# Kernel tuning notes

Hardware: AMD Instinct MI355X
Metric: run time of the kernel (lower is better)

## Reference

```python
import jax, jax.numpy as jnp
import numpy as np
from jax import lax

D_MODEL = 1024
D_STATE = 16
D_CONV = 4
EXPAND = 2
D_INNER = EXPAND * D_MODEL            # 2048
DT_RANK = (D_MODEL + 15) // 16        # 64
B, L = 2, 2048
EPS = 1e-5


def setup_inputs() -> dict:
    key = jax.random.key(0)
    ks = jax.random.split(key, 12)
    s = 0.02
    x = jax.random.normal(ks[0], (B, L, D_MODEL), dtype=jnp.float32)
    norm_w = jnp.ones((D_MODEL,), dtype=jnp.float32)
    in_proj_w = jax.random.normal(ks[1], (2 * D_INNER, D_MODEL), dtype=jnp.float32) * s
    conv_w = jax.random.normal(ks[2], (D_INNER, D_CONV), dtype=jnp.float32) * 0.1
    conv_b = jax.random.normal(ks[3], (D_INNER,), dtype=jnp.float32) * 0.01
    x_proj_w = jax.random.normal(ks[4], (DT_RANK + 2 * D_STATE, D_INNER), dtype=jnp.float32) * s
    dt_proj_w = jax.random.normal(ks[5], (D_INNER, DT_RANK), dtype=jnp.float32) * 0.1
    dt_proj_b = jax.random.normal(ks[6], (D_INNER,), dtype=jnp.float32) * 0.5 - 4.0  # small softplus(delta)
    # S4D-real init: A = -(1..d_state) per channel
    A_log = jnp.log(jnp.broadcast_to(jnp.arange(1, D_STATE + 1, dtype=jnp.float32), (D_INNER, D_STATE)))
    Dp = jnp.ones((D_INNER,), dtype=jnp.float32)
    out_proj_w = jax.random.normal(ks[7], (D_MODEL, D_INNER), dtype=jnp.float32) * s
    return {"x": x, "norm_w": norm_w, "in_proj_w": in_proj_w, "conv_w": conv_w,
            "conv_b": conv_b, "x_proj_w": x_proj_w, "dt_proj_w": dt_proj_w,
            "dt_proj_b": dt_proj_b, "A_log": A_log, "Dp": Dp, "out_proj_w": out_proj_w}


def _selective_scan(deltaA, deltaBu, Cm):
    # deltaA, deltaBu: [B,L,Di,N]; Cm: [B,L,N] -> y: [B,L,Di]
    def step(h, inp):
        dA, dBu, c = inp
        h = dA * h + dBu                       # [B,Di,N]
        y = jnp.einsum('bdn,bn->bd', h, c)     # [B,Di]
        return h, y
    h0 = jnp.zeros(deltaA.shape[0:1] + deltaA.shape[2:], deltaA.dtype)
    _, ys = lax.scan(step, h0, (deltaA.transpose(1, 0, 2, 3),
                                deltaBu.transpose(1, 0, 2, 3),
                                Cm.transpose(1, 0, 2)))
    return ys.transpose(1, 0, 2)               # [B,L,Di]


def reference(x, norm_w, in_proj_w, conv_w, conv_b, x_proj_w,
              dt_proj_w, dt_proj_b, A_log, Dp, out_proj_w):
    d_inner, d_conv = conv_w.shape
    d_state = A_log.shape[1]
    dt_rank = dt_proj_w.shape[1]

    # RMSNorm
    rms = jnp.sqrt(jnp.mean(x * x, axis=-1, keepdims=True) + EPS)
    xn = norm_w * (x / rms)

    # input projection -> x, z streams
    xz = jnp.einsum('bld,ed->ble', xn, in_proj_w)      # [B,L,2*Di]
    xi, z = jnp.split(xz, 2, axis=-1)

    # depthwise causal conv1d + SiLU
    xc = lax.conv_general_dilated(
        xi.transpose(0, 2, 1), conv_w[:, None, :], (1,), [(d_conv - 1, 0)],
        dimension_numbers=('NCL', 'OIL', 'NCL'), feature_group_count=d_inner)
    xc = jax.nn.silu(xc.transpose(0, 2, 1) + conv_b)   # [B,L,Di]

    # input-dependent SSM params
    dbl = jnp.einsum('bld,ed->ble', xc, x_proj_w)      # [B,L,dt_rank+2N]
    dt, Bm, Cm = jnp.split(dbl, [dt_rank, dt_rank + d_state], axis=-1)
    delta = jax.nn.softplus(jnp.einsum('blr,dr->bld', dt, dt_proj_w) + dt_proj_b)

    A = -jnp.exp(A_log)                                # [Di,N]
    deltaA = jnp.exp(delta[..., None] * A)             # [B,L,Di,N]
    deltaBu = delta[..., None] * Bm[:, :, None, :] * xc[..., None]

    y = _selective_scan(deltaA, deltaBu, Cm)           # [B,L,Di]
    y = y + xc * Dp
    y = y * jax.nn.silu(z)

    out = jnp.einsum('bld,ed->ble', y, out_proj_w)     # [B,L,d_model]
    return x + out
```

## Files before the change

kernel.cpp:

```cpp
#include <hip/hip_runtime.h>
#include <hip/hip_bf16.h>
#include <math.h>

#define D_MODEL 1024
#define D_STATE 16
#define D_CONV 4
#define D_INNER 2048
#define DT_RANK 64
#define BATCH 2
#define SEQ 2048
#define NTOK (BATCH*SEQ)
#define EPS 1e-5f
#define CCH 32
#define TCH (SEQ/CCH)
#define XKS 8
#define XKC (D_INNER/XKS)

typedef __attribute__((ext_vector_type(8))) short short8;
typedef __attribute__((ext_vector_type(4))) float f32x4;
typedef __attribute__((ext_vector_type(4))) unsigned short us4;

__device__ inline unsigned short f2bf(float f) {
  union { __hip_bfloat16 h; unsigned short u; } c;
  c.h = __float2bfloat16(f);
  return c.u;
}
__device__ inline float bf2f(unsigned short u) {
  union { unsigned int i; float f; } c;
  c.i = ((unsigned int)u) << 16;
  return c.f;
}

#define GLL(gp, lp) __builtin_amdgcn_global_load_lds( \
    (const __attribute__((address_space(1))) void*)(gp), \
    (__attribute__((address_space(3))) void*)(lp), 16, 0, 0)

__global__ __launch_bounds__(256) void f2bf4_kernel(
    const float* __restrict__ i0, unsigned short* __restrict__ o0, int b0,
    const float* __restrict__ i1, unsigned short* __restrict__ o1, int b1,
    const float* __restrict__ i2, unsigned short* __restrict__ o2, int b2,
    const float* __restrict__ i3, unsigned short* __restrict__ o3)
{
  int blk = blockIdx.x;
  const float* in; unsigned short* out; int base;
  if (blk < b0)           { in = i0; out = o0; base = blk; }
  else if (blk < b0+b1)   { in = i1; out = o1; base = blk - b0; }
  else if (blk < b0+b1+b2){ in = i2; out = o2; base = blk - b0 - b1; }
  else                    { in = i3; out = o3; base = blk - b0 - b1 - b2; }
  int i = (base*256 + threadIdx.x)*4;
  float4 v = *(const float4*)(in + i);
  us4 o;
  o[0] = f2bf(v.x); o[1] = f2bf(v.y); o[2] = f2bf(v.z); o[3] = f2bf(v.w);
  *(us4*)(out + i) = o;
}

__global__ __launch_bounds__(256) void rmsnorm_kernel(const float* __restrict__ x,
                                                      const float* __restrict__ w,
                                                      unsigned short* __restrict__ xn) {
  int tok = blockIdx.x;
  const float* xr = x + (size_t)tok * D_MODEL;
  unsigned short* xo = xn + (size_t)tok * D_MODEL;
  int t = threadIdx.x;
  float4 v = ((const float4*)xr)[t];
  float ss = v.x*v.x + v.y*v.y + v.z*v.z + v.w*v.w;
  #pragma unroll
  for (int off = 32; off > 0; off >>= 1) ss += __shfl_down(ss, off, 64);
  __shared__ float wsum[4];
  __shared__ float rinv_s;
  int lane = t & 63, wv = t >> 6;
  if (lane == 0) wsum[wv] = ss;
  __syncthreads();
  if (t == 0) {
    float tot = wsum[0] + wsum[1] + wsum[2] + wsum[3];
    rinv_s = 1.0f / sqrtf(tot / (float)D_MODEL + EPS);
  }
  __syncthreads();
  float rinv = rinv_s;
  float4 g = ((const float4*)w)[t];
  us4 o;
  o[0] = f2bf(v.x * rinv * g.x);
  o[1] = f2bf(v.y * rinv * g.y);
  o[2] = f2bf(v.z * rinv * g.z);
  o[3] = f2bf(v.w * rinv * g.w);
  *(us4*)(xo + t*4) = o;
}

template<int NT>
__global__ __launch_bounds__(512) void gemm256_bf16_kernel(
    const unsigned short* __restrict__ A,
    const unsigned short* __restrict__ W,
    unsigned short* __restrict__ C, int ldc)
{
  const int K = NT*64;
  __shared__ __align__(16) unsigned short As[2][16384];
  __shared__ __align__(16) unsigned short Bs[2][16384];
  int tid = threadIdx.x;
  int lane = tid & 63;
  int w = tid >> 6;
  int wm = w >> 2, wn = w & 3;
  int bm = blockIdx.x * 256;
  int bn = blockIdx.y * 256;
  int r15 = lane & 15, g8 = (lane >> 4) * 8;
  int rbh0 = (w & 3) + (w >> 2) * 8;
  int rbh1 = rbh0 + 4;

  auto stageA = [&](int slot, int tile, int ks, int rb) {
    const unsigned short* src = A + (size_t)(bm + rb*16 + r15) * K + tile*64 + ks*32 + g8;
    GLL(src, &As[slot][rb*1024 + ks*512]);
  };
  auto stageB = [&](int slot, int tile, int ks, int cb) {
    const unsigned short* src = W + (size_t)(bn + cb*16 + r15) * K + tile*64 + ks*32 + g8;
    GLL(src, &Bs[slot][cb*1024 + ks*512]);
  };

  stageA(0,0,0,rbh0); stageB(0,0,0,w); stageB(0,0,0,8+w);
  stageA(0,0,0,rbh1);
  stageA(0,0,1,rbh0); stageB(0,0,1,w); stageB(0,0,1,8+w);
  stageA(0,0,1,rbh1);
  stageA(1,1,0,rbh0); stageB(1,1,0,w); stageB(1,1,0,8+w);
  stageA(1,1,0,rbh1);
  stageA(1,1,1,rbh0); stageB(1,1,1,w); stageB(1,1,1,8+w);
  asm volatile("s_waitcnt vmcnt(7)" ::: "memory");
  __builtin_amdgcn_s_barrier();
  __builtin_amdgcn_sched_barrier(0);

  f32x4 acc[8][4] = {};
  short8 bfr[4];

#define PHASE_END()                                                      \
  if (drain) { asm volatile("s_waitcnt vmcnt(0)" ::: "memory"); }        \
  else       { asm volatile("s_waitcnt vmcnt(12)" ::: "memory"); }       \
  __builtin_amdgcn_s_barrier();                                          \
  __builtin_amdgcn_sched_barrier(0);

#define MFMA16(IH)                                                       \
  __builtin_amdgcn_s_setprio(1);                                         \
  _Pragma("unroll")                                                      \
  for (int ii = 0; ii < 4; ++ii) {                                       \
    _Pragma("unroll")                                                    \
    for (int j = 0; j < 4; ++j)                                          \
      acc[(IH)*4+ii][j] = __builtin_amdgcn_mfma_f32_16x16x32_bf16(       \
          af[ii], bfr[j], acc[(IH)*4+ii][j], 0, 0, 0);                   \
  }                                                                      \
  __builtin_amdgcn_s_setprio(0);

#define LOAD_A(KS, IH)                                                   \
  short8 af[4];                                                          \
  _Pragma("unroll")                                                      \
  for (int ii = 0; ii < 4; ++ii)                                         \
    af[ii] = *(const short8*)&As[s][(wm*8 + (IH)*4 + ii)*1024 + (KS)*512 + lane*8];

#define LOAD_B(KS)                                                       \
  _Pragma("unroll")                                                      \
  for (int j = 0; j < 4; ++j)                                            \
    bfr[j] = *(const short8*)&Bs[s][(wn*4 + j)*1024 + (KS)*512 + lane*8];

  for (int t = 0; t < NT; ++t) {
    int s = t & 1;
    const bool drain = (t >= NT-2);
    {
      LOAD_A(0,0)
      LOAD_B(0)
      if (t+1 < NT) { stageA(s^1, t+1, 1, rbh1); }
      MFMA16(0)
      PHASE_END()
    }
    {
      LOAD_A(0,1)
      if (t+2 < NT) { stageA(s, t+2, 0, rbh0); stageB(s, t+2, 0, w); stageB(s, t+2, 0, 8+w); }
      MFMA16(1)
      PHASE_END()
    }
    {
      LOAD_A(1,0)
      LOAD_B(1)
      if (t+2 < NT) { stageA(s, t+2, 0, rbh1); }
      MFMA16(0)
      PHASE_END()
    }
    {
      LOAD_A(1,1)
      if (t+2 < NT) { stageA(s, t+2, 1, rbh0); stageB(s, t+2, 1, w); stageB(s, t+2, 1, 8+w); }
      MFMA16(1)
      PHASE_END()
    }
  }
#undef PHASE_END
#undef MFMA16
#undef LOAD_A
#undef LOAD_B

  #pragma unroll
  for (int ig = 0; ig < 8; ++ig) {
    #pragma unroll
    for (int j = 0; j < 4; ++j) {
      #pragma unroll
      for (int r = 0; r < 4; ++r) {
        int row = bm + wm*128 + ig*16 + (lane >> 4)*4 + r;
        int col = bn + wn*64 + j*16 + r15;
        C[(size_t)row * ldc + col] = f2bf(acc[ig][j][r]);
      }
    }
  }
}

template<int EPI, int OBF>
__global__ __launch_bounds__(256) void gemm_bf16_kernel(
    const unsigned short* __restrict__ A,
    const unsigned short* __restrict__ W,
    void* __restrict__ Cv, int ldc, int K,
    const float* __restrict__ resid)
{
  __shared__ __align__(16) unsigned short Abuf[8*64*8];
  __shared__ __align__(16) unsigned short Bbuf[8*64*8];
  int tid = threadIdx.x;
  int lane = tid & 63;
  int w = tid >> 6;
  int bm = blockIdx.x * 128;
  int bn = blockIdx.y * 128;
  int wrow = (w >> 1) * 64;
  int wcol = (w & 1) * 64;

  int r15 = lane & 15, g = lane >> 4;
  const unsigned short* Ag0 = A + (size_t)(bm + 2*w*16 + r15) * K + g*8;
  const unsigned short* Ag1 = Ag0 + (size_t)16 * K;
  const unsigned short* Wg0 = W + (size_t)(bn + 2*w*16 + r15) * K + g*8;
  const unsigned short* Wg1 = Wg0 + (size_t)16 * K;
  unsigned short* Al0 = &Abuf[(2*w  )*512];
  unsigned short* Al1 = &Abuf[(2*w+1)*512];
  unsigned short* Bl0 = &Bbuf[(2*w  )*512];
  unsigned short* Bl1 = &Bbuf[(2*w+1)*512];

  f32x4 acc[4][4] = {};

  for (int k0 = 0; k0 < K; k0 += 32) {
    __syncthreads();
    GLL(Ag0 + k0, Al0);
    GLL(Ag1 + k0, Al1);
    GLL(Wg0 + k0, Bl0);
    GLL(Wg1 + k0, Bl1);
    __syncthreads();

    short8 af[4], bfr[4];
    #pragma unroll
    for (int i = 0; i < 4; ++i)
      af[i] = *(const short8*)&Abuf[((wrow >> 4) + i)*512 + lane*8];
    #pragma unroll
    for (int j = 0; j < 4; ++j)
      bfr[j] = *(const short8*)&Bbuf[((wcol >> 4) + j)*512 + lane*8];
    #pragma unroll
    for (int i = 0; i < 4; ++i)
      #pragma unroll
      for (int j = 0; j < 4; ++j)
        acc[i][j] = __builtin_amdgcn_mfma_f32_16x16x32_bf16(af[i], bfr[j], acc[i][j], 0, 0, 0);
  }

  #pragma unroll
  for (int i = 0; i < 4; ++i) {
    #pragma unroll
    for (int j = 0; j < 4; ++j) {
      #pragma unroll
      for (int r = 0; r < 4; ++r) {
        int row = bm + wrow + i*16 + (lane >> 4)*4 + r;
        int col = bn + wcol + j*16 + (lane & 15);
        float v = acc[i][j][r];
        if (EPI == 2) v += resid[(size_t)row * ldc + col];
        if (OBF) ((unsigned short*)Cv)[(size_t)row * ldc + col] = f2bf(v);
        else     ((float*)Cv)[(size_t)row * ldc + col] = v;
      }
    }
  }
}

__global__ __launch_bounds__(256) void xproj_bf16_kernel(
    const unsigned short* __restrict__ A,
    const unsigned short* __restrict__ W,
    float* __restrict__ Ppart)
{
  __shared__ __align__(16) unsigned short Abuf[8*512];
  __shared__ __align__(16) unsigned short Bbuf[6*512];
  int tid = threadIdx.x;
  int lane = tid & 63;
  int w = tid >> 6;
  int bm = blockIdx.x * 128;
  int kc = blockIdx.y;
  const int K = D_INNER;
  int r15 = lane & 15, g = lane >> 4;

  const unsigned short* Ag0 = A + (size_t)(bm + 2*w*16 + r15) * K + g*8 + kc*XKC;
  const unsigned short* Ag1 = Ag0 + (size_t)16 * K;
  const unsigned short* Wg0 = W + (size_t)(w*16 + r15) * K + g*8 + kc*XKC;
  const unsigned short* Wg1 = W + (size_t)((4+w)*16 + r15) * K + g*8 + kc*XKC;
  unsigned short* Al0 = &Abuf[(2*w  )*512];
  unsigned short* Al1 = &Abuf[(2*w+1)*512];
  unsigned short* Bl0 = &Bbuf[w*512];
  unsigned short* Bl1 = &Bbuf[(4+w)*512];

  f32x4 acc[2][6] = {};

  for (int k0 = 0; k0 < XKC; k0 += 32) {
    __syncthreads();
    GLL(Ag0 + k0, Al0);
    GLL(Ag1 + k0, Al1);
    GLL(Wg0 + k0, Bl0);
    if (w < 2) GLL(Wg1 + k0, Bl1);
    __syncthreads();

    short8 af[2], bfr[6];
    #pragma unroll
    for (int i = 0; i < 2; ++i)
      af[i] = *(const short8*)&Abuf[(2*w + i)*512 + lane*8];
    #pragma unroll
    for (int j = 0; j < 6; ++j)
      bfr[j] = *(const short8*)&Bbuf[j*512 + lane*8];
    #pragma unroll
    for (int i = 0; i < 2; ++i)
      #pragma unroll
      for (int j = 0; j < 6; ++j)
        acc[i][j] = __builtin_amdgcn_mfma_f32_16x16x32_bf16(af[i], bfr[j], acc[i][j], 0, 0, 0);
  }

  float* out = Ppart + (size_t)kc * NTOK * 96;
  #pragma unroll
  for (int i = 0; i < 2; ++i) {
    #pragma unroll
    for (int j = 0; j < 6; ++j) {
      #pragma unroll
      for (int r = 0; r < 4; ++r) {
        int row = bm + w*32 + i*16 + (lane >> 4)*4 + r;
        int col = j*16 + (lane & 15);
        out[(size_t)row * 96 + col] = acc[i][j][r];
      }
    }
  }
}

__global__ __launch_bounds__(256) void xproj_reduce_kernel(
    const float* __restrict__ Ppart, float* __restrict__ dbl)
{
  int idx = blockIdx.x * 256 + threadIdx.x;
  float s = 0.f;
  #pragma unroll
  for (int k = 0; k < XKS; ++k) s += Ppart[(size_t)k * NTOK * 96 + idx];
  dbl[idx] = s;
}

__global__ __launch_bounds__(256) void dtproj_kernel(
    const float* __restrict__ dbl,
    const unsigned short* __restrict__ Wdt,
    const float* __restrict__ bias,
    unsigned short* __restrict__ delta)
{
  __shared__ unsigned short Wl[256*68];
  __shared__ float dts[16][64];
  int tid = threadIdx.x;
  int dBase = blockIdx.x * 256;
  int tok0 = blockIdx.y * 16;

  #pragma unroll
  for (int i = 0; i < 8; ++i) {
    int idx = i*256 + tid;
    int row = idx >> 3, kc = (idx & 7) * 8;
    const us4* src = (const us4*)(Wdt + (size_t)(dBase + row)*64 + kc);
    us4 lo = src[0], hi = src[1];
    *(us4*)&Wl[row*68 + kc    ] = lo;
    *(us4*)&Wl[row*68 + kc + 4] = hi;
  }
  {
    int t = tid >> 4, kq = tid & 15;
    *(float4*)&dts[t][kq*4] = *(const float4*)(dbl + (size_t)(tok0 + t)*96 + kq*4);
  }
  __syncthreads();

  int d = dBase + tid;
  float s[16];
  float bd = bias[d];
  #pragma unroll
  for (int t = 0; t < 16; ++t) s[t] = bd;

  #pragma unroll
  for (int j = 0; j < 16; ++j) {
    us4 wv = *(const us4*)&Wl[tid*68 + j*4];
    float w0 = bf2f(wv[0]), w1 = bf2f(wv[1]), w2 = bf2f(wv[2]), w3 = bf2f(wv[3]);
    #pragma unroll
    for (int t = 0; t < 16; ++t) {
      float4 dv = *(const float4*)&dts[t][j*4];
      s[t] = fmaf(dv.x, w0, s[t]);
      s[t] = fmaf(dv.y, w1, s[t]);
      s[t] = fmaf(dv.z, w2, s[t]);
      s[t] = fmaf(dv.w, w3, s[t]);
    }
  }

  #pragma unroll
  for (int t = 0; t < 16; ++t) {
    float v = s[t];
    float sp = (v > 20.f) ? v : __logf(1.f + __expf(v));
    delta[(size_t)(tok0 + t) * D_INNER + d] = f2bf(sp);
  }
}

__global__ __launch_bounds__(256) void conv_silu_kernel(
    const unsigned short* __restrict__ xz, const float* __restrict__ cw,
    const float* __restrict__ cb, unsigned short* __restrict__ xcbf)
{
  int idx = blockIdx.x * 256 + threadIdx.x;
  int dq = idx & (D_INNER/4 - 1);
  int tok = idx >> 9;
  int l = tok & (SEQ - 1);
  int d = dq * 4;
  const unsigned short* xi = xz + (size_t)tok * (2*D_INNER) + d;
  us4 v3 = *(const us4*)xi;
  us4 v2 = l >= 1 ? *(const us4*)(xi - 1*(2*D_INNER)) : (us4)0;
  us4 v1 = l >= 2 ? *(const us4*)(xi - 2*(2*D_INNER)) : (us4)0;
  us4 v0 = l >= 3 ? *(const us4*)(xi - 3*(2*D_INNER)) : (us4)0;
  float4 cbv = *(const float4*)(cb + d);
  float cbx[4] = {cbv.x, cbv.y, cbv.z, cbv.w};
  us4 o;
  #pragma unroll
  for (int j = 0; j < 4; ++j) {
    float4 wv = *(const float4*)(cw + (d + j) * 4);
    float s = cbx[j];
    s = fmaf(bf2f(v0[j]), wv.x, s);
    s = fmaf(bf2f(v1[j]), wv.y, s);
    s = fmaf(bf2f(v2[j]), wv.z, s);
    s = fmaf(bf2f(v3[j]), wv.w, s);
    float v = s / (1.f + __expf(-s));
    o[j] = f2bf(v);
  }
  *(us4*)(xcbf + (size_t)tok * D_INNER + d) = o;
}

__global__ __launch_bounds__(256) void scan_pass1(
    const unsigned short* __restrict__ delta, const float* __restrict__ dbl,
    const unsigned short* __restrict__ xc, const float* __restrict__ A_log,
    float* __restrict__ P, float* __restrict__ He)
{
  int blk = blockIdx.x;
  int d = (blk & 7) * 256 + threadIdx.x;
  int c = (blk >> 3) & (CCH - 1);
  int b = blk >> 8;
  float Adn[16];
  #pragma unroll
  for (int n = 0; n < 16; ++n) Adn[n] = -__expf(A_log[d*16 + n]);
  float h[16] = {};
  float sdl = 0.f;
  int tok0 = b * SEQ + c * TCH;
  for (int t = 0; t < TCH; ++t) {
    size_t tok = (size_t)(tok0 + t);
    float dl = bf2f(delta[tok * D_INNER + d]);
    float xcv = bf2f(xc[tok * D_INNER + d]);
    float u = dl * xcv;
    const float4* bp = (const float4*)(dbl + tok*96 + 64);
    float4 b0 = bp[0], b1 = bp[1], b2 = bp[2], b3 = bp[3];
    float bv[16] = {b0.x,b0.y,b0.z,b0.w, b1.x,b1.y,b1.z,b1.w,
                    b2.x,b2.y,b2.z,b2.w, b3.x,b3.y,b3.z,b3.w};
    sdl += dl;
    #pragma unroll
    for (int n = 0; n < 16; ++n)
      h[n] = fmaf(__expf(dl * Adn[n]), h[n], u * bv[n]);
  }
  size_t base = ((size_t)(b*CCH + c) * 16) * D_INNER + d;
  #pragma unroll
  for (int n = 0; n < 16; ++n) {
    P [base + (size_t)n * D_INNER] = __expf(Adn[n] * sdl);
    He[base + (size_t)n * D_INNER] = h[n];
  }
}

__global__ __launch_bounds__(256) void scan_pass2(
    const float* __restrict__ P, const float* __restrict__ He,
    float* __restrict__ Hin)
{
  int blk = blockIdx.x;
  int d = (blk & 7) * 256 + threadIdx.x;
  int n = (blk >> 3) & 15;
  int b = blk >> 7;
  float h = 0.f;
  #pragma unroll 4
  for (int c = 0; c < CCH; ++c) {
    size_t idx = ((size_t)(b*CCH + c) * 16 + n) * D_INNER + d;
    Hin[idx] = h;
    h = fmaf(P[idx], h, He[idx]);
  }
}

__global__ __launch_bounds__(256) void scan_pass3(
    const unsigned short* __restrict__ delta, const float* __restrict__ dbl,
    const unsigned short* __restrict__ xc, const unsigned short* __restrict__ xz,
    const float* __restrict__ A_log, const float* __restrict__ Dp,
    const float* __restrict__ Hin, unsigned short* __restrict__ y)
{
  int blk = blockIdx.x;
  int d = (blk & 7) * 256 + threadIdx.x;
  int c = (blk >> 3) & (CCH - 1);
  int b = blk >> 8;
  float Adn[16];
  #pragma unroll
  for (int n = 0; n < 16; ++n) Adn[n] = -__expf(A_log[d*16 + n]);
  float Dpd = Dp[d];
  float h[16];
  size_t base = ((size_t)(b*CCH + c) * 16) * D_INNER + d;
  #pragma unroll
  for (int n = 0; n < 16; ++n) h[n] = Hin[base + (size_t)n * D_INNER];
  int tok0 = b * SEQ + c * TCH;
  for (int t = 0; t < TCH; ++t) {
    size_t tok = (size_t)(tok0 + t);
    float dl = bf2f(delta[tok * D_INNER + d]);
    float xcv = bf2f(xc[tok * D_INNER + d]);
    float u = dl * xcv;
    const float4* bp = (const float4*)(dbl + tok*96 + 64);
    float4 b0 = bp[0], b1 = bp[1], b2 = bp[2], b3 = bp[3];
    float4 c0 = bp[4], c1 = bp[5], c2 = bp[6], c3 = bp[7];
    float bv[16] = {b0.x,b0.y,b0.z,b0.w, b1.x,b1.y,b1.z,b1.w,
                    b2.x,b2.y,b2.z,b2.w, b3.x,b3.y,b3.z,b3.w};
    float cv[16] = {c0.x,c0.y,c0.z,c0.w, c1.x,c1.y,c1.z,c1.w,
                    c2.x,c2.y,c2.z,c2.w, c3.x,c3.y,c3.z,c3.w};
    float z = bf2f(xz[tok * (2*D_INNER) + D_INNER + d]);
    float acc = xcv * Dpd;
    #pragma unroll
    for (int n = 0; n < 16; ++n) {
      h[n] = fmaf(__expf(dl * Adn[n]), h[n], u * bv[n]);
      acc = fmaf(h[n], cv[n], acc);
    }
    float sz = z / (1.f + __expf(-z));
    y[tok * D_INNER + d] = f2bf(acc * sz);
  }
}

extern "C" void kernel_launch(void* const* d_in, const int* in_sizes, int n_in,
                              void* d_out, int out_size, void* d_ws, size_t ws_size,
                              hipStream_t stream) {
  const float* x         = (const float*)d_in[0];
  const float* norm_w    = (const float*)d_in[1];
  const float* in_proj_w = (const float*)d_in[2];
  const float* conv_w    = (const float*)d_in[3];
  const float* conv_b    = (const float*)d_in[4];
  const float* x_proj_w  = (const float*)d_in[5];
  const float* dt_proj_w = (const float*)d_in[6];
  const float* dt_proj_b = (const float*)d_in[7];
  const float* A_log     = (const float*)d_in[8];
  const float* Dp        = (const float*)d_in[9];
  const float* out_proj_w= (const float*)d_in[10];
  float* out = (float*)d_out;

  char* ws = (char*)d_ws;
  unsigned short* xz_bf   = (unsigned short*)(ws);
  unsigned short* xc_bf   = (unsigned short*)(ws + ( 32ull<<20));
  float*          dbl     = (float*)(ws + ( 48ull<<20));
  unsigned short* delta_bf= (unsigned short*)(ws + ( 50ull<<20));
  unsigned short* xn_bf   = (unsigned short*)(ws + ( 66ull<<20));
  unsigned short* w_in_bf = (unsigned short*)(ws + ( 74ull<<20));
  unsigned short* w_out_bf= (unsigned short*)(ws + ( 82ull<<20));
  unsigned short* w_xp_bf = (unsigned short*)(ws + ( 86ull<<20));
  unsigned short* w_dt_bf = (unsigned short*)(ws + ( 87ull<<20));
  float*          Ppart   = (float*)(ws + ( 89ull<<20));
  float*          Pst     = (float*)(ws + (102ull<<20));
  float*          Hest    = (float*)(ws + (110ull<<20));
  float*          Hin     = (float*)(ws + (118ull<<20));
  unsigned short* yb_bf   = (unsigned short*)(ws + (126ull<<20));

  rmsnorm_kernel<<<NTOK, 256, 0, stream>>>(x, norm_w, xn_bf);

  f2bf4_kernel<<<4096+2048+192+128, 256, 0, stream>>>(
      in_proj_w, w_in_bf, 4096,
      out_proj_w, w_out_bf, 2048,
      x_proj_w, w_xp_bf, 192,
      dt_proj_w, w_dt_bf);

  {
    dim3 g(NTOK/256, (2*D_INNER)/256);
    gemm256_bf16_kernel<D_MODEL/64><<<g, 512, 0, stream>>>(xn_bf, w_in_bf, xz_bf, 2*D_INNER);
  }

  conv_silu_kernel<<<(NTOK*D_INNER/4)/256, 256, 0, stream>>>(xz_bf, conv_w, conv_b, xc_bf);

  {
    dim3 g(NTOK/128, XKS);
    xproj_bf16_kernel<<<g, 256, 0, stream>>>(xc_bf, w_xp_bf, Ppart);
    xproj_reduce_kernel<<<(NTOK*96)/256, 256, 0, stream>>>(Ppart, dbl);
  }

  {
    dim3 g(D_INNER/256, NTOK/16);
    dtproj_kernel<<<g, 256, 0, stream>>>(dbl, w_dt_bf, dt_proj_b, delta_bf);
  }

  scan_pass1<<<BATCH*CCH*8, 256, 0, stream>>>(delta_bf, dbl, xc_bf, A_log, Pst, Hest);
  scan_pass2<<<BATCH*16*8, 256, 0, stream>>>(Pst, Hest, Hin);
  scan_pass3<<<BATCH*CCH*8, 256, 0, stream>>>(delta_bf, dbl, xc_bf, xz_bf, A_log, Dp, Hin, yb_bf);

  {
    dim3 g(NTOK/128, D_MODEL/128);
    gemm_bf16_kernel<2,0><<<g, 256, 0, stream>>>(yb_bf, w_out_bf, out, D_MODEL, D_INNER, x);
  }
}
```

Measured before the change: 365.0 us.

## Use split-K 256-tile GEMM for out_proj with separate residual reduce

Replaces the 128x128 single-buffered out_proj GEMM with the pipelined 256x256 GEMM kernel, split four ways along K so the grid has 256 blocks. Each K-slice writes fp32 partials into reused workspace regions, and a new reduce kernel sums them with the residual. This aims to raise MFMA efficiency and occupancy for the out_proj. In exchange it adds about 64MB of extra partial-sum traffic and one more kernel launch.

```diff
diff --git a/kernel.cpp b/kernel.cpp
--- a/kernel.cpp
+++ b/kernel.cpp
@@ -85,13 +85,13 @@
   *(us4*)(xo + t*4) = o;
 }
 
-template<int NT>
+template<int NT, int OBF>
 __global__ __launch_bounds__(512) void gemm256_bf16_kernel(
     const unsigned short* __restrict__ A,
     const unsigned short* __restrict__ W,
-    unsigned short* __restrict__ C, int ldc)
-{
-  const int K = NT*64;
+    void* __restrict__ Cv, int ldc, int lda,
+    float* __restrict__ P1, float* __restrict__ P2, float* __restrict__ P3)
+{
   __shared__ __align__(16) unsigned short As[2][16384];
   __shared__ __align__(16) unsigned short Bs[2][16384];
   int tid = threadIdx.x;
@@ -100,16 +100,18 @@
   int wm = w >> 2, wn = w & 3;
   int bm = blockIdx.x * 256;
   int bn = blockIdx.y * 256;
+  int kc = blockIdx.z;
+  int koff = kc * (NT*64);
   int r15 = lane & 15, g8 = (lane >> 4) * 8;
   int rbh0 = (w & 3) + (w >> 2) * 8;
   int rbh1 = rbh0 + 4;
 
   auto stageA = [&](int slot, int tile, int ks, int rb) {
-    const unsigned short* src = A + (size_t)(bm + rb*16 + r15) * K + tile*64 + ks*32 + g8;
+    const unsigned short* src = A + (size_t)(bm + rb*16 + r15) * lda + koff + tile*64 + ks*32 + g8;
     GLL(src, &As[slot][rb*1024 + ks*512]);
   };
   auto stageB = [&](int slot, int tile, int ks, int cb) {
-    const unsigned short* src = W + (size_t)(bn + cb*16 + r15) * K + tile*64 + ks*32 + g8;
+    const unsigned short* src = W + (size_t)(bn + cb*16 + r15) * lda + koff + tile*64 + ks*32 + g8;
     GLL(src, &Bs[slot][cb*1024 + ks*512]);
   };
 
@@ -190,6 +192,8 @@
 #undef LOAD_A
 #undef LOAD_B
 
+  float* fout;
+  if (OBF == 0) fout = (kc == 0) ? (float*)Cv : (kc == 1) ? P1 : (kc == 2) ? P2 : P3;
   #pragma unroll
   for (int ig = 0; ig < 8; ++ig) {
     #pragma unroll
@@ -198,78 +202,30 @@
       for (int r = 0; r < 4; ++r) {
         int row = bm + wm*128 + ig*16 + (lane >> 4)*4 + r;
         int col = bn + wn*64 + j*16 + r15;
-        C[(size_t)row * ldc + col] = f2bf(acc[ig][j][r]);
+        if (OBF) ((unsigned short*)Cv)[(size_t)row * ldc + col] = f2bf(acc[ig][j][r]);
+        else     fout[(size_t)row * ldc + col] = acc[ig][j][r];
       }
     }
   }
 }
 
-template<int EPI, int OBF>
-__global__ __launch_bounds__(256) void gemm_bf16_kernel(
-    const unsigned short* __restrict__ A,
-    const unsigned short* __restrict__ W,
-    void* __restrict__ Cv, int ldc, int K,
-    const float* __restrict__ resid)
-{
-  __shared__ __align__(16) unsigned short Abuf[8*64*8];
-  __shared__ __align__(16) unsigned short Bbuf[8*64*8];
-  int tid = threadIdx.x;
-  int lane = tid & 63;
-  int w = tid >> 6;
-  int bm = blockIdx.x * 128;
-  int bn = blockIdx.y * 128;
-  int wrow = (w >> 1) * 64;
-  int wcol = (w & 1) * 64;
-
-  int r15 = lane & 15, g = lane >> 4;
-  const unsigned short* Ag0 = A + (size_t)(bm + 2*w*16 + r15) * K + g*8;
-  const unsigned short* Ag1 = Ag0 + (size_t)16 * K;
-  const unsigned short* Wg0 = W + (size_t)(bn + 2*w*16 + r15) * K + g*8;
-  const unsigned short* Wg1 = Wg0 + (size_t)16 * K;
-  unsigned short* Al0 = &Abuf[(2*w  )*512];
-  unsigned short* Al1 = &Abuf[(2*w+1)*512];
-  unsigned short* Bl0 = &Bbuf[(2*w  )*512];
-  unsigned short* Bl1 = &Bbuf[(2*w+1)*512];
-
-  f32x4 acc[4][4] = {};
-
-  for (int k0 = 0; k0 < K; k0 += 32) {
-    __syncthreads();
-    GLL(Ag0 + k0, Al0);
-    GLL(Ag1 + k0, Al1);
-    GLL(Wg0 + k0, Bl0);
-    GLL(Wg1 + k0, Bl1);
-    __syncthreads();
-
-    short8 af[4], bfr[4];
-    #pragma unroll
-    for (int i = 0; i < 4; ++i)
-      af[i] = *(const short8*)&Abuf[((wrow >> 4) + i)*512 + lane*8];
-    #pragma unroll
-    for (int j = 0; j < 4; ++j)
-      bfr[j] = *(const short8*)&Bbuf[((wcol >> 4) + j)*512 + lane*8];
-    #pragma unroll
-    for (int i = 0; i < 4; ++i)
-      #pragma unroll
-      for (int j = 0; j < 4; ++j)
-        acc[i][j] = __builtin_amdgcn_mfma_f32_16x16x32_bf16(af[i], bfr[j], acc[i][j], 0, 0, 0);
-  }
-
-  #pragma unroll
-  for (int i = 0; i < 4; ++i) {
-    #pragma unroll
-    for (int j = 0; j < 4; ++j) {
-      #pragma unroll
-      for (int r = 0; r < 4; ++r) {
-        int row = bm + wrow + i*16 + (lane >> 4)*4 + r;
-        int col = bn + wcol + j*16 + (lane & 15);
-        float v = acc[i][j][r];
-        if (EPI == 2) v += resid[(size_t)row * ldc + col];
-        if (OBF) ((unsigned short*)Cv)[(size_t)row * ldc + col] = f2bf(v);
-        else     ((float*)Cv)[(size_t)row * ldc + col] = v;
-      }
-    }
-  }
+__global__ __launch_bounds__(256) void outproj_reduce_kernel(
+    const float* __restrict__ p0, const float* __restrict__ p1,
+    const float* __restrict__ p2, const float* __restrict__ p3,
+    const float* __restrict__ x, float* __restrict__ out)
+{
+  int i = (blockIdx.x * 256 + threadIdx.x) * 4;
+  float4 a = *(const float4*)(p0 + i);
+  float4 b = *(const float4*)(p1 + i);
+  float4 c = *(const float4*)(p2 + i);
+  float4 d = *(const float4*)(p3 + i);
+  float4 r = *(const float4*)(x + i);
+  float4 o;
+  o.x = r.x + a.x + b.x + c.x + d.x;
+  o.y = r.y + a.y + b.y + c.y + d.y;
+  o.z = r.z + a.z + b.z + c.z + d.z;
+  o.w = r.w + a.w + b.w + c.w + d.w;
+  *(float4*)(out + i) = o;
 }
 
 __global__ __launch_bounds__(256) void xproj_bf16_kernel(
@@ -559,6 +515,10 @@
   float*          Hest    = (float*)(ws + (110ull<<20));
   float*          Hin     = (float*)(ws + (118ull<<20));
   unsigned short* yb_bf   = (unsigned short*)(ws + (126ull<<20));
+  float*          OP0     = (float*)(ws + ( 50ull<<20));
+  float*          OP1     = (float*)(ws + ( 66ull<<20));
+  float*          OP2     = (float*)(ws + ( 89ull<<20));
+  float*          OP3     = (float*)(ws + (105ull<<20));
 
   rmsnorm_kernel<<<NTOK, 256, 0, stream>>>(x, norm_w, xn_bf);
 
@@ -569,8 +529,9 @@
       dt_proj_w, w_dt_bf);
 
   {
-    dim3 g(NTOK/256, (2*D_INNER)/256);
-    gemm256_bf16_kernel<D_MODEL/64><<<g, 512, 0, stream>>>(xn_bf, w_in_bf, xz_bf, 2*D_INNER);
+    dim3 g(NTOK/256, (2*D_INNER)/256, 1);
+    gemm256_bf16_kernel<D_MODEL/64, 1><<<g, 512, 0, stream>>>(
+        xn_bf, w_in_bf, xz_bf, 2*D_INNER, D_MODEL, nullptr, nullptr, nullptr);
   }
 
   conv_silu_kernel<<<(NTOK*D_INNER/4)/256, 256, 0, stream>>>(xz_bf, conv_w, conv_b, xc_bf);
@@ -591,7 +552,9 @@
   scan_pass3<<<BATCH*CCH*8, 256, 0, stream>>>(delta_bf, dbl, xc_bf, xz_bf, A_log, Dp, Hin, yb_bf);
 
   {
-    dim3 g(NTOK/128, D_MODEL/128);
-    gemm_bf16_kernel<2,0><<<g, 256, 0, stream>>>(yb_bf, w_out_bf, out, D_MODEL, D_INNER, x);
-  }
-}
+    dim3 g(NTOK/256, D_MODEL/256, 4);
+    gemm256_bf16_kernel<(D_INNER/4)/64, 0><<<g, 512, 0, stream>>>(
+        yb_bf, w_out_bf, OP0, D_MODEL, D_INNER, OP1, OP2, OP3);
+    outproj_reduce_kernel<<<(NTOK*D_MODEL/4)/256, 256, 0, stream>>>(OP0, OP1, OP2, OP3, x, out);
+  }
+}
```

Result: faster. 345.2 us (-5.4%).
